# Kernel tuning notes

Measured on AMD Instinct MI355X. Metric: run time of the kernel, lower is better.

Reference implementation:

```python
import jax, jax.numpy as jnp
import numpy as np

B, T, D_IN, H = 1024, 512, 32, 64


def setup_inputs() -> dict:
    key = jax.random.key(0)
    ks = jax.random.split(key, 16)
    s_in = 1.0 / np.sqrt(H)  # torch LSTM init scale 1/sqrt(hidden)
    inp = {
        "x": jax.random.normal(ks[0], (B, T, D_IN), dtype=jnp.float32),
        # layer 0
        "Wih0": jax.random.uniform(ks[1], (4 * H, D_IN), minval=-s_in, maxval=s_in),
        "Whh0": jax.random.uniform(ks[2], (4 * H, H), minval=-s_in, maxval=s_in),
        "bih0": jax.random.uniform(ks[3], (4 * H,), minval=-s_in, maxval=s_in),
        "bhh0": jax.random.uniform(ks[4], (4 * H,), minval=-s_in, maxval=s_in),
        # layer 1
        "Wih1": jax.random.uniform(ks[5], (4 * H, H), minval=-s_in, maxval=s_in),
        "Whh1": jax.random.uniform(ks[6], (4 * H, H), minval=-s_in, maxval=s_in),
        "bih1": jax.random.uniform(ks[7], (4 * H,), minval=-s_in, maxval=s_in),
        "bhh1": jax.random.uniform(ks[8], (4 * H,), minval=-s_in, maxval=s_in),
        # head: Linear(H, H//2) -> ReLU -> Linear(H//2, 1)
        "W1": jax.random.uniform(ks[9], (H // 2, H), minval=-s_in, maxval=s_in),
        "b1": jax.random.uniform(ks[10], (H // 2,), minval=-s_in, maxval=s_in),
        "W2": jax.random.uniform(ks[11], (1, H // 2), minval=-1.0 / np.sqrt(H // 2), maxval=1.0 / np.sqrt(H // 2)),
        "b2": jax.random.uniform(ks[12], (1,), minval=-1.0 / np.sqrt(H // 2), maxval=1.0 / np.sqrt(H // 2)),
    }
    return inp


def _lstm_layer(x, Wih, Whh, bih, bhh):
    # x: [B, T, D]; returns all hidden states [B, T, H]
    b = x.shape[0]
    xT = jnp.swapaxes(x, 0, 1)  # [T, B, D]
    h0 = jnp.zeros((b, H), dtype=x.dtype)
    c0 = jnp.zeros((b, H), dtype=x.dtype)
    bias = bih + bhh

    def step(carry, xt):
        h, c = carry
        z = xt @ Wih.T + h @ Whh.T + bias  # [B, 4H]
        i, f, g, o = jnp.split(z, 4, axis=-1)  # torch gate order: i, f, g, o
        i = jax.nn.sigmoid(i)
        f = jax.nn.sigmoid(f)
        g = jnp.tanh(g)
        o = jax.nn.sigmoid(o)
        c = f * c + i * g
        h = o * jnp.tanh(c)
        return (h, c), h

    _, hs = jax.lax.scan(step, (h0, c0), xT)
    return jnp.swapaxes(hs, 0, 1)  # [B, T, H]


def reference(x, Wih0, Whh0, bih0, bhh0, Wih1, Whh1, bih1, bhh1, W1, b1, W2, b2):
    h1 = _lstm_layer(x, Wih0, Whh0, bih0, bhh0)   # [B, T, H]
    h2 = _lstm_layer(h1, Wih1, Whh1, bih1, bhh1)  # [B, T, H] (dropout = identity, eval)
    last = h2[:, -1]                              # [B, H]
    hidden = jax.nn.relu(last @ W1.T + b1)        # [B, H//2]
    out = hidden @ W2.T + b2                      # [B, 1]
    return out[:, 0]                              # [B]
```

## Files before the change

### kernel.cpp

```cpp
#include <hip/hip_runtime.h>

#define T       512
#define DIN     32
#define HCELLS  64
#define NB      16
#define TB      512
#define GRID    64

typedef _Float16 half8  __attribute__((ext_vector_type(8)));
typedef _Float16 half4v __attribute__((ext_vector_type(4)));
typedef _Float16 half2v __attribute__((ext_vector_type(2)));
typedef float    float4v __attribute__((ext_vector_type(4)));

#define STRX    40
#define STRH    72
#define XH_OFF  0
#define H0H_OFF (2*16*STRX)
#define H1H_OFF (H0H_OFF + 2*16*STRH)
#define SB_HALFS (H1H_OFF + 2*16*STRH)

#define LOG2E   1.44269504f
#define SLOG2E  2.88539008f

__device__ __forceinline__ int xidx(int p, int n, int k) { return (p * 16 + n) * STRX + k; }
__device__ __forceinline__ int hidx(int p, int n, int k) { return (p * 16 + n) * STRH + k; }

__device__ __forceinline__ void cvt8(const float* v, half8& hi) {
    #pragma unroll
    for (int e = 0; e < 8; ++e) hi[e] = (_Float16)v[e];
}

__device__ __forceinline__ void cell_update(const float4v acc[4], float* cs,
                                            half4v& hh, float* hout)
{
    #pragma unroll
    for (int r = 0; r < 4; ++r) {
        float ei = __builtin_amdgcn_exp2f(acc[0][r]);
        float ef = __builtin_amdgcn_exp2f(acc[1][r]);
        float G2 = __builtin_amdgcn_exp2f(acc[2][r]);
        float I  = 1.0f + ei, F = 1.0f + ef;
        float Gp = 1.0f + G2;
        float Gms = fmaf(SLOG2E, G2, -SLOG2E);
        float P   = I * Gp;
        float num = fmaf(F, Gms, cs[r] * P);
        float csn = num * __builtin_amdgcn_rcpf(F * P);
        csn = fminf(fmaxf(csn, -50.0f), 50.0f);
        cs[r] = csn;
        float eo = __builtin_amdgcn_exp2f(acc[3][r]);
        float C2 = __builtin_amdgcn_exp2f(csn);
        float O  = 1.0f + eo;
        float Cp = 1.0f + C2, Cm = C2 - 1.0f;
        float h  = Cm * __builtin_amdgcn_rcpf(O * Cp);
        if (hout) hout[r] = h;
        hh[r] = (_Float16)h;
    }
}

__global__ void __launch_bounds__(TB, 2)
lstm2_mfma_kernel(const float* __restrict__ x,
                  const float* __restrict__ Wih0, const float* __restrict__ Whh0,
                  const float* __restrict__ bih0, const float* __restrict__ bhh0,
                  const float* __restrict__ Wih1, const float* __restrict__ Whh1,
                  const float* __restrict__ bih1, const float* __restrict__ bhh1,
                  const float* __restrict__ W1,   const float* __restrict__ b1,
                  const float* __restrict__ W2,   const float* __restrict__ b2,
                  float* __restrict__ out)
{
    const int tid  = threadIdx.x;
    const int wid  = tid >> 6;
    const int grp  = wid >> 2;
    const int wl   = wid & 3;
    const int lane = tid & 63;
    const int n16  = lane & 15;
    const int q    = lane >> 4;
    const int j0   = wl * 16 + q * 4;
    const int b0   = blockIdx.x * NB;

    __shared__ __align__(16) _Float16 SB[SB_HALFS];
    __shared__ __align__(16) float HS[16 * 68 + 16 * 33];

    const float gsc[4] = {-LOG2E, -LOG2E, SLOG2E, -LOG2E};

    half8 ah[4][4];
    float4v biasv[4];

    #pragma unroll
    for (int l = 0; l < 4; ++l) {
        const int row = (l * 4 + wl) * 16 + n16;
        const float g = gsc[l];
        float v[8];
        if (grp == 0) {
            {
                const float4* p = (const float4*)(Wih0 + row * DIN + q * 8);
                float4 u0 = p[0], u1 = p[1];
                v[0]=g*u0.x; v[1]=g*u0.y; v[2]=g*u0.z; v[3]=g*u0.w;
                v[4]=g*u1.x; v[5]=g*u1.y; v[6]=g*u1.z; v[7]=g*u1.w;
                cvt8(v, ah[l][0]);
            }
            #pragma unroll
            for (int kt = 1; kt < 3; ++kt) {
                const float4* p = (const float4*)(Whh0 + row * HCELLS + (kt - 1) * 32 + q * 8);
                float4 u0 = p[0], u1 = p[1];
                v[0]=g*u0.x; v[1]=g*u0.y; v[2]=g*u0.z; v[3]=g*u0.w;
                v[4]=g*u1.x; v[5]=g*u1.y; v[6]=g*u1.z; v[7]=g*u1.w;
                cvt8(v, ah[l][kt]);
            }
            const int r0 = l * 64 + j0;
            float4v bi = *(const float4v*)(bih0 + r0);
            float4v bh = *(const float4v*)(bhh0 + r0);
            biasv[l] = (bi + bh) * g;
        } else {
            #pragma unroll
            for (int kt = 0; kt < 4; ++kt) {
                const float* base = (kt < 2) ? (Wih1 + row * HCELLS + kt * 32)
                                             : (Whh1 + row * HCELLS + (kt - 2) * 32);
                const float4* p = (const float4*)(base + q * 8);
                float4 u0 = p[0], u1 = p[1];
                v[0]=g*u0.x; v[1]=g*u0.y; v[2]=g*u0.z; v[3]=g*u0.w;
                v[4]=g*u1.x; v[5]=g*u1.y; v[6]=g*u1.z; v[7]=g*u1.w;
                cvt8(v, ah[l][kt]);
            }
            const int r0 = l * 64 + j0;
            float4v bi = *(const float4v*)(bih1 + r0);
            float4v bh = *(const float4v*)(bhh1 + r0);
            biasv[l] = (bi + bh) * g;
        }
    }

    for (int i = tid; i < SB_HALFS / 2; i += TB) ((int*)SB)[i] = 0;

    const int nx = tid >> 4;
    const int kp = (tid & 15) * 2;
    const float* xp0 = (grp == 0) ? (x + (size_t)(b0 + nx) * T * DIN + kp) : nullptr;
    __syncthreads();
    if (grp == 0) {
        float2 xv = *(const float2*)xp0;
        half2v hi = {(_Float16)xv.x, (_Float16)xv.y};
        *(half2v*)&SB[XH_OFF + xidx(0, nx, kp)] = hi;
    }
    __syncthreads();

    float cs[4] = {0, 0, 0, 0};
    float hlast[4];
    const float* xp = (grp == 0) ? (xp0 + DIN) : nullptr;

    #pragma unroll 2
    for (int t = 0; t < T; ++t) {
        const int pr = t & 1, pw = pr ^ 1;

        if (grp == 0) {
            float2 xv;
            const bool havex = (t + 1 < T);
            if (havex) xv = *(const float2*)xp;
            xp += DIN;

            float4v acc[4];
            #pragma unroll
            for (int l = 0; l < 4; ++l) acc[l] = biasv[l];
            {
                half8 bh = *(const half8*)&SB[XH_OFF + xidx(pr, n16, q * 8)];
                #pragma unroll
                for (int l = 0; l < 4; ++l)
                    acc[l] = __builtin_amdgcn_mfma_f32_16x16x32_f16(ah[l][0], bh, acc[l], 0, 0, 0);
            }
            #pragma unroll
            for (int kt = 1; kt < 3; ++kt) {
                half8 bh = *(const half8*)&SB[H0H_OFF + hidx(pr, n16, (kt - 1) * 32 + q * 8)];
                #pragma unroll
                for (int l = 0; l < 4; ++l)
                    acc[l] = __builtin_amdgcn_mfma_f32_16x16x32_f16(ah[l][kt], bh, acc[l], 0, 0, 0);
            }
            half4v hh;
            cell_update(acc, cs, hh, nullptr);
            *(half4v*)&SB[H0H_OFF + hidx(pw, n16, j0)] = hh;
            if (havex) {
                half2v hi = {(_Float16)xv.x, (_Float16)xv.y};
                *(half2v*)&SB[XH_OFF + xidx(pw, nx, kp)] = hi;
            }
        } else if (t > 0) {
            float4v acc[4];
            #pragma unroll
            for (int l = 0; l < 4; ++l) acc[l] = biasv[l];
            #pragma unroll
            for (int kt = 0; kt < 4; ++kt) {
                half8 bh = (kt < 2)
                    ? *(const half8*)&SB[H0H_OFF + hidx(pr, n16, kt * 32 + q * 8)]
                    : *(const half8*)&SB[H1H_OFF + hidx(pw, n16, (kt - 2) * 32 + q * 8)];
                #pragma unroll
                for (int l = 0; l < 4; ++l)
                    acc[l] = __builtin_amdgcn_mfma_f32_16x16x32_f16(ah[l][kt], bh, acc[l], 0, 0, 0);
            }
            half4v hh;
            cell_update(acc, cs, hh, nullptr);
            *(half4v*)&SB[H1H_OFF + hidx(pr, n16, j0)] = hh;
        }
        __syncthreads();
    }

    float* h1f = HS;
    float* hid = HS + 16 * 68;
    if (grp == 1) {
        float4v acc[4];
        #pragma unroll
        for (int l = 0; l < 4; ++l) acc[l] = biasv[l];
        #pragma unroll
        for (int kt = 0; kt < 4; ++kt) {
            half8 bh = (kt < 2)
                ? *(const half8*)&SB[H0H_OFF + hidx(0, n16, kt * 32 + q * 8)]
                : *(const half8*)&SB[H1H_OFF + hidx(1, n16, (kt - 2) * 32 + q * 8)];
            #pragma unroll
            for (int l = 0; l < 4; ++l)
                acc[l] = __builtin_amdgcn_mfma_f32_16x16x32_f16(ah[l][kt], bh, acc[l], 0, 0, 0);
        }
        half4v hh;
        cell_update(acc, cs, hh, hlast);
        *(float4*)&h1f[n16 * 68 + j0] = *(const float4*)hlast;
    }
    __syncthreads();

    if (tid < 256) {
        const int n2 = tid >> 4, m = tid & 15;
        float s0 = b1[m], s1 = b1[m + 16];
        const float* w0p = W1 + m * HCELLS;
        const float* w1p = W1 + (m + 16) * HCELLS;
        #pragma unroll
        for (int j = 0; j < HCELLS; ++j) {
            float hv = h1f[n2 * 68 + j];
            s0 = fmaf(w0p[j], hv, s0);
            s1 = fmaf(w1p[j], hv, s1);
        }
        hid[n2 * 33 + m]      = fmaxf(s0, 0.0f);
        hid[n2 * 33 + m + 16] = fmaxf(s1, 0.0f);
    }
    __syncthreads();

    if (tid < NB) {
        float s = b2[0];
        #pragma unroll
        for (int m = 0; m < 32; ++m) s = fmaf(W2[m], hid[tid * 33 + m], s);
        out[b0 + tid] = s;
    }
}

extern "C" void kernel_launch(void* const* d_in, const int* in_sizes, int n_in,
                              void* d_out, int out_size, void* d_ws, size_t ws_size,
                              hipStream_t stream) {
    const float* x    = (const float*)d_in[0];
    const float* Wih0 = (const float*)d_in[1];
    const float* Whh0 = (const float*)d_in[2];
    const float* bih0 = (const float*)d_in[3];
    const float* bhh0 = (const float*)d_in[4];
    const float* Wih1 = (const float*)d_in[5];
    const float* Whh1 = (const float*)d_in[6];
    const float* bih1 = (const float*)d_in[7];
    const float* bhh1 = (const float*)d_in[8];
    const float* W1   = (const float*)d_in[9];
    const float* b1   = (const float*)d_in[10];
    const float* W2   = (const float*)d_in[11];
    const float* b2   = (const float*)d_in[12];
    float* out = (float*)d_out;

    hipLaunchKernelGGL(lstm2_mfma_kernel, dim3(GRID), dim3(TB), 0, stream,
                       x, Wih0, Whh0, bih0, bhh0, Wih1, Whh1, bih1, bhh1,
                       W1, b1, W2, b2, out);
}
```

Before: 452.0 us.

## Merge both LSTM layers into each wave and load x directly into registers

Each block drops from 8 waves (4 per layer) to 4 waves, and every wave now computes both layer-0 and layer-1 gates for its slice. The layer-1 MFMAs are interleaved with the layer-0 ones. The input x is prefetched straight into registers as an MFMA B operand instead of being staged through shared memory, which removes the x LDS writes and reads. The intent is to shorten the per-step barrier with fewer waves and to give each wave independent MFMA chains that hide latency. The costs are more registers per thread and serial work per wave, launch bounds changed to 1, and less wave-level parallelism per CU.

```diff
diff --git a/kernel.cpp b/kernel.cpp
--- a/kernel.cpp
+++ b/kernel.cpp
@@ -4,25 +4,21 @@
 #define DIN     32
 #define HCELLS  64
 #define NB      16
-#define TB      512
+#define TB      256
 #define GRID    64
 
 typedef _Float16 half8  __attribute__((ext_vector_type(8)));
 typedef _Float16 half4v __attribute__((ext_vector_type(4)));
-typedef _Float16 half2v __attribute__((ext_vector_type(2)));
 typedef float    float4v __attribute__((ext_vector_type(4)));
 
-#define STRX    40
 #define STRH    72
-#define XH_OFF  0
-#define H0H_OFF (2*16*STRX)
-#define H1H_OFF (H0H_OFF + 2*16*STRH)
+#define H0H_OFF 0
+#define H1H_OFF (2*16*STRH)
 #define SB_HALFS (H1H_OFF + 2*16*STRH)
 
 #define LOG2E   1.44269504f
 #define SLOG2E  2.88539008f
 
-__device__ __forceinline__ int xidx(int p, int n, int k) { return (p * 16 + n) * STRX + k; }
 __device__ __forceinline__ int hidx(int p, int n, int k) { return (p * 16 + n) * STRH + k; }
 
 __device__ __forceinline__ void cvt8(const float* v, half8& hi) {
@@ -56,7 +52,7 @@
     }
 }
 
-__global__ void __launch_bounds__(TB, 2)
+__global__ void __launch_bounds__(TB, 1)
 lstm2_mfma_kernel(const float* __restrict__ x,
                   const float* __restrict__ Wih0, const float* __restrict__ Whh0,
                   const float* __restrict__ bih0, const float* __restrict__ bhh0,
@@ -67,9 +63,7 @@
                   float* __restrict__ out)
 {
     const int tid  = threadIdx.x;
-    const int wid  = tid >> 6;
-    const int grp  = wid >> 2;
-    const int wl   = wid & 3;
+    const int wl   = tid >> 6;
     const int lane = tid & 63;
     const int n16  = lane & 15;
     const int q    = lane >> 4;
@@ -81,144 +75,145 @@
 
     const float gsc[4] = {-LOG2E, -LOG2E, SLOG2E, -LOG2E};
 
-    half8 ah[4][4];
-    float4v biasv[4];
+    half8 ah0[4][3];
+    half8 ah1[4][4];
+    float4v biasv0[4], biasv1[4];
 
     #pragma unroll
     for (int l = 0; l < 4; ++l) {
         const int row = (l * 4 + wl) * 16 + n16;
         const float g = gsc[l];
         float v[8];
-        if (grp == 0) {
-            {
-                const float4* p = (const float4*)(Wih0 + row * DIN + q * 8);
-                float4 u0 = p[0], u1 = p[1];
-                v[0]=g*u0.x; v[1]=g*u0.y; v[2]=g*u0.z; v[3]=g*u0.w;
-                v[4]=g*u1.x; v[5]=g*u1.y; v[6]=g*u1.z; v[7]=g*u1.w;
-                cvt8(v, ah[l][0]);
-            }
-            #pragma unroll
-            for (int kt = 1; kt < 3; ++kt) {
-                const float4* p = (const float4*)(Whh0 + row * HCELLS + (kt - 1) * 32 + q * 8);
-                float4 u0 = p[0], u1 = p[1];
-                v[0]=g*u0.x; v[1]=g*u0.y; v[2]=g*u0.z; v[3]=g*u0.w;
-                v[4]=g*u1.x; v[5]=g*u1.y; v[6]=g*u1.z; v[7]=g*u1.w;
-                cvt8(v, ah[l][kt]);
-            }
+        {
+            const float4* p = (const float4*)(Wih0 + row * DIN + q * 8);
+            float4 u0 = p[0], u1 = p[1];
+            v[0]=g*u0.x; v[1]=g*u0.y; v[2]=g*u0.z; v[3]=g*u0.w;
+            v[4]=g*u1.x; v[5]=g*u1.y; v[6]=g*u1.z; v[7]=g*u1.w;
+            cvt8(v, ah0[l][0]);
+        }
+        #pragma unroll
+        for (int kt = 1; kt < 3; ++kt) {
+            const float4* p = (const float4*)(Whh0 + row * HCELLS + (kt - 1) * 32 + q * 8);
+            float4 u0 = p[0], u1 = p[1];
+            v[0]=g*u0.x; v[1]=g*u0.y; v[2]=g*u0.z; v[3]=g*u0.w;
+            v[4]=g*u1.x; v[5]=g*u1.y; v[6]=g*u1.z; v[7]=g*u1.w;
+            cvt8(v, ah0[l][kt]);
+        }
+        {
             const int r0 = l * 64 + j0;
             float4v bi = *(const float4v*)(bih0 + r0);
             float4v bh = *(const float4v*)(bhh0 + r0);
-            biasv[l] = (bi + bh) * g;
-        } else {
-            #pragma unroll
-            for (int kt = 0; kt < 4; ++kt) {
-                const float* base = (kt < 2) ? (Wih1 + row * HCELLS + kt * 32)
-                                             : (Whh1 + row * HCELLS + (kt - 2) * 32);
-                const float4* p = (const float4*)(base + q * 8);
-                float4 u0 = p[0], u1 = p[1];
-                v[0]=g*u0.x; v[1]=g*u0.y; v[2]=g*u0.z; v[3]=g*u0.w;
-                v[4]=g*u1.x; v[5]=g*u1.y; v[6]=g*u1.z; v[7]=g*u1.w;
-                cvt8(v, ah[l][kt]);
-            }
+            biasv0[l] = (bi + bh) * g;
+        }
+        #pragma unroll
+        for (int kt = 0; kt < 4; ++kt) {
+            const float* base = (kt < 2) ? (Wih1 + row * HCELLS + kt * 32)
+                                         : (Whh1 + row * HCELLS + (kt - 2) * 32);
+            const float4* p = (const float4*)(base + q * 8);
+            float4 u0 = p[0], u1 = p[1];
+            v[0]=g*u0.x; v[1]=g*u0.y; v[2]=g*u0.z; v[3]=g*u0.w;
+            v[4]=g*u1.x; v[5]=g*u1.y; v[6]=g*u1.z; v[7]=g*u1.w;
+            cvt8(v, ah1[l][kt]);
+        }
+        {
             const int r0 = l * 64 + j0;
             float4v bi = *(const float4v*)(bih1 + r0);
             float4v bh = *(const float4v*)(bhh1 + r0);
-            biasv[l] = (bi + bh) * g;
+            biasv1[l] = (bi + bh) * g;
         }
     }
 
     for (int i = tid; i < SB_HALFS / 2; i += TB) ((int*)SB)[i] = 0;
 
-    const int nx = tid >> 4;
-    const int kp = (tid & 15) * 2;
-    const float* xp0 = (grp == 0) ? (x + (size_t)(b0 + nx) * T * DIN + kp) : nullptr;
+    const float* xq = x + ((size_t)(b0 + n16) * T) * DIN + q * 8;
+    float4 xn0 = *(const float4*)xq;
+    float4 xn1 = *(const float4*)(xq + 4);
+    xq += DIN;
+
     __syncthreads();
-    if (grp == 0) {
-        float2 xv = *(const float2*)xp0;
-        half2v hi = {(_Float16)xv.x, (_Float16)xv.y};
-        *(half2v*)&SB[XH_OFF + xidx(0, nx, kp)] = hi;
-    }
-    __syncthreads();
-
-    float cs[4] = {0, 0, 0, 0};
+
+    float cs0[4] = {0, 0, 0, 0};
+    float cs1[4] = {0, 0, 0, 0};
     float hlast[4];
-    const float* xp = (grp == 0) ? (xp0 + DIN) : nullptr;
+
+    {
+        float4 xc0 = xn0, xc1 = xn1;
+        xn0 = *(const float4*)xq; xn1 = *(const float4*)(xq + 4); xq += DIN;
+        half8 bhx;
+        bhx[0]=(_Float16)xc0.x; bhx[1]=(_Float16)xc0.y; bhx[2]=(_Float16)xc0.z; bhx[3]=(_Float16)xc0.w;
+        bhx[4]=(_Float16)xc1.x; bhx[5]=(_Float16)xc1.y; bhx[6]=(_Float16)xc1.z; bhx[7]=(_Float16)xc1.w;
+        float4v acc0[4];
+        #pragma unroll
+        for (int l = 0; l < 4; ++l)
+            acc0[l] = __builtin_amdgcn_mfma_f32_16x16x32_f16(ah0[l][0], bhx, biasv0[l], 0, 0, 0);
+        half4v hh0;
+        cell_update(acc0, cs0, hh0, nullptr);
+        *(half4v*)&SB[H0H_OFF + hidx(1, n16, j0)] = hh0;
+        __syncthreads();
+    }
 
     #pragma unroll 2
-    for (int t = 0; t < T; ++t) {
+    for (int t = 1; t < T; ++t) {
         const int pr = t & 1, pw = pr ^ 1;
 
-        if (grp == 0) {
-            float2 xv;
-            const bool havex = (t + 1 < T);
-            if (havex) xv = *(const float2*)xp;
-            xp += DIN;
-
-            float4v acc[4];
-            #pragma unroll
-            for (int l = 0; l < 4; ++l) acc[l] = biasv[l];
-            {
-                half8 bh = *(const half8*)&SB[XH_OFF + xidx(pr, n16, q * 8)];
-                #pragma unroll
-                for (int l = 0; l < 4; ++l)
-                    acc[l] = __builtin_amdgcn_mfma_f32_16x16x32_f16(ah[l][0], bh, acc[l], 0, 0, 0);
-            }
-            #pragma unroll
-            for (int kt = 1; kt < 3; ++kt) {
-                half8 bh = *(const half8*)&SB[H0H_OFF + hidx(pr, n16, (kt - 1) * 32 + q * 8)];
-                #pragma unroll
-                for (int l = 0; l < 4; ++l)
-                    acc[l] = __builtin_amdgcn_mfma_f32_16x16x32_f16(ah[l][kt], bh, acc[l], 0, 0, 0);
-            }
-            half4v hh;
-            cell_update(acc, cs, hh, nullptr);
-            *(half4v*)&SB[H0H_OFF + hidx(pw, n16, j0)] = hh;
-            if (havex) {
-                half2v hi = {(_Float16)xv.x, (_Float16)xv.y};
-                *(half2v*)&SB[XH_OFF + xidx(pw, nx, kp)] = hi;
-            }
-        } else if (t > 0) {
-            float4v acc[4];
-            #pragma unroll
-            for (int l = 0; l < 4; ++l) acc[l] = biasv[l];
-            #pragma unroll
-            for (int kt = 0; kt < 4; ++kt) {
-                half8 bh = (kt < 2)
-                    ? *(const half8*)&SB[H0H_OFF + hidx(pr, n16, kt * 32 + q * 8)]
-                    : *(const half8*)&SB[H1H_OFF + hidx(pw, n16, (kt - 2) * 32 + q * 8)];
-                #pragma unroll
-                for (int l = 0; l < 4; ++l)
-                    acc[l] = __builtin_amdgcn_mfma_f32_16x16x32_f16(ah[l][kt], bh, acc[l], 0, 0, 0);
-            }
-            half4v hh;
-            cell_update(acc, cs, hh, nullptr);
-            *(half4v*)&SB[H1H_OFF + hidx(pr, n16, j0)] = hh;
-        }
+        float4 xc0 = xn0, xc1 = xn1;
+        if (t + 1 < T) { xn0 = *(const float4*)xq; xn1 = *(const float4*)(xq + 4); xq += DIN; }
+
+        half8 bhx;
+        bhx[0]=(_Float16)xc0.x; bhx[1]=(_Float16)xc0.y; bhx[2]=(_Float16)xc0.z; bhx[3]=(_Float16)xc0.w;
+        bhx[4]=(_Float16)xc1.x; bhx[5]=(_Float16)xc1.y; bhx[6]=(_Float16)xc1.z; bhx[7]=(_Float16)xc1.w;
+
+        half8 bh0a = *(const half8*)&SB[H0H_OFF + hidx(pr, n16, q * 8)];
+        half8 bh0b = *(const half8*)&SB[H0H_OFF + hidx(pr, n16, 32 + q * 8)];
+        half8 bh1a = *(const half8*)&SB[H1H_OFF + hidx(pw, n16, q * 8)];
+        half8 bh1b = *(const half8*)&SB[H1H_OFF + hidx(pw, n16, 32 + q * 8)];
+
+        float4v acc0[4], acc1[4];
+        #pragma unroll
+        for (int l = 0; l < 4; ++l) {
+            acc0[l] = __builtin_amdgcn_mfma_f32_16x16x32_f16(ah0[l][0], bhx,  biasv0[l], 0, 0, 0);
+            acc1[l] = __builtin_amdgcn_mfma_f32_16x16x32_f16(ah1[l][0], bh0a, biasv1[l], 0, 0, 0);
+        }
+        #pragma unroll
+        for (int l = 0; l < 4; ++l) {
+            acc0[l] = __builtin_amdgcn_mfma_f32_16x16x32_f16(ah0[l][1], bh0a, acc0[l], 0, 0, 0);
+            acc0[l] = __builtin_amdgcn_mfma_f32_16x16x32_f16(ah0[l][2], bh0b, acc0[l], 0, 0, 0);
+            acc1[l] = __builtin_amdgcn_mfma_f32_16x16x32_f16(ah1[l][1], bh0b, acc1[l], 0, 0, 0);
+            acc1[l] = __builtin_amdgcn_mfma_f32_16x16x32_f16(ah1[l][2], bh1a, acc1[l], 0, 0, 0);
+            acc1[l] = __builtin_amdgcn_mfma_f32_16x16x32_f16(ah1[l][3], bh1b, acc1[l], 0, 0, 0);
+        }
+
+        half4v hh0, hh1;
+        cell_update(acc0, cs0, hh0, nullptr);
+        cell_update(acc1, cs1, hh1, nullptr);
+        *(half4v*)&SB[H0H_OFF + hidx(pw, n16, j0)] = hh0;
+        *(half4v*)&SB[H1H_OFF + hidx(pr, n16, j0)] = hh1;
         __syncthreads();
     }
 
     float* h1f = HS;
     float* hid = HS + 16 * 68;
-    if (grp == 1) {
+    {
+        half8 bh0a = *(const half8*)&SB[H0H_OFF + hidx(0, n16, q * 8)];
+        half8 bh0b = *(const half8*)&SB[H0H_OFF + hidx(0, n16, 32 + q * 8)];
+        half8 bh1a = *(const half8*)&SB[H1H_OFF + hidx(1, n16, q * 8)];
+        half8 bh1b = *(const half8*)&SB[H1H_OFF + hidx(1, n16, 32 + q * 8)];
         float4v acc[4];
         #pragma unroll
-        for (int l = 0; l < 4; ++l) acc[l] = biasv[l];
-        #pragma unroll
-        for (int kt = 0; kt < 4; ++kt) {
-            half8 bh = (kt < 2)
-                ? *(const half8*)&SB[H0H_OFF + hidx(0, n16, kt * 32 + q * 8)]
-                : *(const half8*)&SB[H1H_OFF + hidx(1, n16, (kt - 2) * 32 + q * 8)];
-            #pragma unroll
-            for (int l = 0; l < 4; ++l)
-                acc[l] = __builtin_amdgcn_mfma_f32_16x16x32_f16(ah[l][kt], bh, acc[l], 0, 0, 0);
+        for (int l = 0; l < 4; ++l) {
+            acc[l] = __builtin_amdgcn_mfma_f32_16x16x32_f16(ah1[l][0], bh0a, biasv1[l], 0, 0, 0);
+            acc[l] = __builtin_amdgcn_mfma_f32_16x16x32_f16(ah1[l][1], bh0b, acc[l], 0, 0, 0);
+            acc[l] = __builtin_amdgcn_mfma_f32_16x16x32_f16(ah1[l][2], bh1a, acc[l], 0, 0, 0);
+            acc[l] = __builtin_amdgcn_mfma_f32_16x16x32_f16(ah1[l][3], bh1b, acc[l], 0, 0, 0);
         }
         half4v hh;
-        cell_update(acc, cs, hh, hlast);
-        *(float4*)&h1f[n16 * 68 + j0] = *(const float4*)hlast;
+        cell_update(acc, cs1, hh, hlast);
+        #pragma unroll
+        for (int r = 0; r < 4; ++r) h1f[n16 * 68 + j0 + r] = hlast[r];
     }
     __syncthreads();
 
-    if (tid < 256) {
+    {
         const int n2 = tid >> 4, m = tid & 15;
         float s0 = b1[m], s1 = b1[m + 16];
         const float* w0p = W1 + m * HCELLS;
```

After: 611.9 us. +35.4%, slower.

## Load x directly into MFMA B-fragment registers and use a lighter barrier

Applied to the files above, without the earlier changes.

Each layer-0 lane now loads its own eight x values straight from global memory into registers, one step ahead, and converts them to an f16 MFMA operand. This removes the shared-memory staging of x and the extra LDS write and read each timestep. The per-step __syncthreads is replaced by an inline-asm s_waitcnt lgkmcnt(0) plus s_barrier, which does not wait for outstanding global loads, so the x prefetch can overlap the barrier. Each lane now reads 32 bytes per step with a stride of T*DIN between rows, which may coalesce less well than the old 16-thread cooperative loads.

```diff
diff --git a/kernel.cpp b/kernel.cpp
--- a/kernel.cpp
+++ b/kernel.cpp
@@ -9,20 +9,18 @@
 
 typedef _Float16 half8  __attribute__((ext_vector_type(8)));
 typedef _Float16 half4v __attribute__((ext_vector_type(4)));
-typedef _Float16 half2v __attribute__((ext_vector_type(2)));
 typedef float    float4v __attribute__((ext_vector_type(4)));
 
-#define STRX    40
 #define STRH    72
-#define XH_OFF  0
-#define H0H_OFF (2*16*STRX)
-#define H1H_OFF (H0H_OFF + 2*16*STRH)
+#define H0H_OFF 0
+#define H1H_OFF (2*16*STRH)
 #define SB_HALFS (H1H_OFF + 2*16*STRH)
 
 #define LOG2E   1.44269504f
 #define SLOG2E  2.88539008f
 
-__device__ __forceinline__ int xidx(int p, int n, int k) { return (p * 16 + n) * STRX + k; }
+#define BARRIER() asm volatile("s_waitcnt lgkmcnt(0)\n\ts_barrier" ::: "memory")
+
 __device__ __forceinline__ int hidx(int p, int n, int k) { return (p * 16 + n) * STRH + k; }
 
 __device__ __forceinline__ void cvt8(const float* v, half8& hi) {
@@ -129,40 +127,36 @@
 
     for (int i = tid; i < SB_HALFS / 2; i += TB) ((int*)SB)[i] = 0;
 
-    const int nx = tid >> 4;
-    const int kp = (tid & 15) * 2;
-    const float* xp0 = (grp == 0) ? (x + (size_t)(b0 + nx) * T * DIN + kp) : nullptr;
-    __syncthreads();
+    const float* xq = nullptr;
+    float4 xn0, xn1;
     if (grp == 0) {
-        float2 xv = *(const float2*)xp0;
-        half2v hi = {(_Float16)xv.x, (_Float16)xv.y};
-        *(half2v*)&SB[XH_OFF + xidx(0, nx, kp)] = hi;
-    }
+        xq = x + ((size_t)(b0 + n16) * T) * DIN + q * 8;
+        xn0 = *(const float4*)xq;
+        xn1 = *(const float4*)(xq + 4);
+        xq += DIN;
+    }
+
     __syncthreads();
 
     float cs[4] = {0, 0, 0, 0};
     float hlast[4];
-    const float* xp = (grp == 0) ? (xp0 + DIN) : nullptr;
 
     #pragma unroll 2
     for (int t = 0; t < T; ++t) {
         const int pr = t & 1, pw = pr ^ 1;
 
         if (grp == 0) {
-            float2 xv;
-            const bool havex = (t + 1 < T);
-            if (havex) xv = *(const float2*)xp;
-            xp += DIN;
+            float4 xc0 = xn0, xc1 = xn1;
+            if (t + 1 < T) { xn0 = *(const float4*)xq; xn1 = *(const float4*)(xq + 4); xq += DIN; }
+
+            half8 bhx;
+            bhx[0]=(_Float16)xc0.x; bhx[1]=(_Float16)xc0.y; bhx[2]=(_Float16)xc0.z; bhx[3]=(_Float16)xc0.w;
+            bhx[4]=(_Float16)xc1.x; bhx[5]=(_Float16)xc1.y; bhx[6]=(_Float16)xc1.z; bhx[7]=(_Float16)xc1.w;
 
             float4v acc[4];
             #pragma unroll
-            for (int l = 0; l < 4; ++l) acc[l] = biasv[l];
-            {
-                half8 bh = *(const half8*)&SB[XH_OFF + xidx(pr, n16, q * 8)];
-                #pragma unroll
-                for (int l = 0; l < 4; ++l)
-                    acc[l] = __builtin_amdgcn_mfma_f32_16x16x32_f16(ah[l][0], bh, acc[l], 0, 0, 0);
-            }
+            for (int l = 0; l < 4; ++l)
+                acc[l] = __builtin_amdgcn_mfma_f32_16x16x32_f16(ah[l][0], bhx, biasv[l], 0, 0, 0);
             #pragma unroll
             for (int kt = 1; kt < 3; ++kt) {
                 half8 bh = *(const half8*)&SB[H0H_OFF + hidx(pr, n16, (kt - 1) * 32 + q * 8)];
@@ -173,10 +167,6 @@
             half4v hh;
             cell_update(acc, cs, hh, nullptr);
             *(half4v*)&SB[H0H_OFF + hidx(pw, n16, j0)] = hh;
-            if (havex) {
-                half2v hi = {(_Float16)xv.x, (_Float16)xv.y};
-                *(half2v*)&SB[XH_OFF + xidx(pw, nx, kp)] = hi;
-            }
         } else if (t > 0) {
             float4v acc[4];
             #pragma unroll
@@ -194,7 +184,7 @@
             cell_update(acc, cs, hh, nullptr);
             *(half4v*)&SB[H1H_OFF + hidx(pr, n16, j0)] = hh;
         }
-        __syncthreads();
+        BARRIER();
     }
 
     float* h1f = HS;
```

Measured after the change: 455.0 us. About the same (+0.6%).
